# Optimization experiments

Measured on AMD Instinct MI355X. Metric: run time of the kernel, lower is better.

The kernel has to match this reference:

```python
import jax, jax.numpy as jnp
import numpy as np

B, N, DIM = 1, 4096, 512
HEADS, LOCAL_HEADS = 8, 4           # int(8*0.6)=4 local, 4 content
CONTENT_HEADS = HEADS - LOCAL_HEADS
HEAD_DIM = DIM // HEADS             # 64
WINDOW = 64                         # == H == W so window attention is well-formed
TOPK_RATIO = 0.2
SCALE = HEAD_DIM ** -0.5


def _window_partition(x, ws):
    Bb, H, W, C = x.shape
    pad_h = (ws - H % ws) % ws
    pad_w = (ws - W % ws) % ws
    x = jnp.pad(x, ((0, 0), (0, pad_h), (0, pad_w), (0, 0)))
    Hp, Wp = H + pad_h, W + pad_w
    x = x.reshape(Bb, Hp // ws, ws, Wp // ws, ws, C)
    win = x.transpose(0, 1, 3, 2, 4, 5).reshape(-1, ws, ws, C)
    return win, (Hp, Wp)


def _window_unpartition(win, ws, pad_hw, hw):
    Hp, Wp = pad_hw
    H, W = hw
    Bb = win.shape[0] // (Hp * Wp // ws // ws)
    x = win.reshape(Bb, Hp // ws, Wp // ws, ws, ws, -1)
    x = x.transpose(0, 1, 3, 2, 4, 5).reshape(Bb, Hp, Wp, -1)
    return x[:, :H, :W, :]


def setup_inputs() -> dict:
    key = jax.random.key(0)
    ks = jax.random.split(key, 12)
    s = 0.02
    f32 = jnp.float32
    ld = LOCAL_HEADS * HEAD_DIM      # 256
    cd = CONTENT_HEADS * HEAD_DIM    # 256
    return {
        'x': jax.random.normal(ks[0], (B, N, DIM), f32),
        'W_lqkv': jax.random.normal(ks[1], (DIM, 3 * ld), f32) * s,
        'b_lqkv': jnp.zeros((3 * ld,), f32),
        'W_cqkv': jax.random.normal(ks[2], (DIM, 3 * cd), f32) * s,
        'b_cqkv': jnp.zeros((3 * cd,), f32),
        'W_lproj': jax.random.normal(ks[3], (ld, DIM), f32) * s,
        'b_lproj': jnp.zeros((DIM,), f32),
        'W_cproj': jax.random.normal(ks[4], (cd, DIM), f32) * s,
        'b_cproj': jnp.zeros((DIM,), f32),
        'W_s1': jax.random.normal(ks[5], (DIM, DIM // 2), f32) * s,
        'b_s1': jnp.zeros((DIM // 2,), f32),
        'W_s2': jax.random.normal(ks[6], (DIM // 2, 1), f32) * s,
        'b_s2': jnp.zeros((1,), f32),
    }


def reference(x, W_lqkv, b_lqkv, W_cqkv, b_cqkv, W_lproj, b_lproj,
              W_cproj, b_cproj, W_s1, b_s1, W_s2, b_s2):
    Bb, Nn, C = x.shape
    H = W = int(np.sqrt(Nn))

    # ---- local (windowed) attention branch ----
    x_sp = x.reshape(Bb, H, W, C)
    x_win, pad_hw = _window_partition(x_sp, WINDOW)           # (Bw, ws, ws, C)
    Bw, Hw, Ww, _ = x_win.shape
    Nw = Hw * Ww
    xl = x_win.reshape(Bw, Nw, C)
    lqkv = (xl @ W_lqkv + b_lqkv).reshape(Bw, Nw, 3, LOCAL_HEADS, HEAD_DIM)
    lqkv = lqkv.transpose(2, 0, 3, 1, 4)                      # (3, Bw, h, Nw, d)
    lq, lk, lv = lqkv[0], lqkv[1], lqkv[2]
    lattn = jnp.einsum('bhqd,bhkd->bhqk', lq, lk) * SCALE
    lattn = jax.nn.softmax(lattn, axis=-1)
    lo = jnp.einsum('bhqk,bhkd->bhqd', lattn, lv)
    lo = lo.transpose(0, 2, 1, 3).reshape(Bw, Hw, Ww, LOCAL_HEADS * HEAD_DIM)
    lo = _window_unpartition(lo, WINDOW, pad_hw, (H, W)).reshape(Bb, Nn, -1)
    local_x = lo @ W_lproj + b_lproj

    # ---- saliency-gated content-based sparse attention branch ----
    h = jax.nn.gelu(x @ W_s1 + b_s1, approximate=False)
    scores = (h @ W_s2 + b_s2)[..., 0]                        # (B, N)
    K = max(1, int(Nn * TOPK_RATIO))
    _, idx = jax.lax.top_k(scores, K)                         # (B, K)
    mask = jnp.zeros((Bb, Nn), bool).at[jnp.arange(Bb)[:, None], idx].set(True)

    cqkv = (x @ W_cqkv + b_cqkv).reshape(Bb, Nn, 3, CONTENT_HEADS, HEAD_DIM)
    cqkv = cqkv.transpose(2, 0, 3, 1, 4)
    cq, ck, cv = cqkv[0], cqkv[1], cqkv[2]
    cattn = jnp.einsum('bhqd,bhkd->bhqk', cq, ck) * SCALE
    cattn = jnp.where(mask[:, None, None, :], cattn, -jnp.inf)
    cattn = jax.nn.softmax(cattn, axis=-1)
    co = jnp.einsum('bhqk,bhkd->bhqd', cattn, cv)
    co = co.transpose(0, 2, 1, 3).reshape(Bb, Nn, CONTENT_HEADS * HEAD_DIM)
    content_x = co @ W_cproj + b_cproj

    out = local_x + content_x
    attn = jnp.concatenate([lattn.mean(axis=1), cattn.mean(axis=1)], axis=1)
    return out, attn
```

## Files before the change

kernel.cpp:

```cpp
#include <hip/hip_runtime.h>

typedef __bf16 bf16;
typedef __bf16 bf16x4 __attribute__((ext_vector_type(4)));
typedef __bf16 bf16x8 __attribute__((ext_vector_type(8)));
typedef float  floatx4 __attribute__((ext_vector_type(4)));

__device__ __forceinline__ floatx4 mfma16(bf16x8 a, bf16x8 b, floatx4 c) {
    return __builtin_amdgcn_mfma_f32_16x16x32_bf16(a, b, c, 0, 0, 0);
}

__device__ __forceinline__ void transpose_tile(const float* __restrict__ src,
                                               bf16* __restrict__ dst,
                                               int R, int C, int rt, int ct,
                                               float (*tile)[33]) {
    int t = threadIdx.x;
    int tx = t & 31, ty = t >> 5;
    int c0 = ct * 32, r0 = rt * 32;
    for (int i = ty; i < 32; i += 8) {
        int r = r0 + i, c = c0 + tx;
        tile[i][tx] = (r < R && c < C) ? src[r * C + c] : 0.f;
    }
    __syncthreads();
    for (int i = ty; i < 32; i += 8) {
        int r = r0 + tx, c = c0 + i;
        if (r < R && c < C) dst[(size_t)c * R + r] = (bf16)tile[tx][i];
    }
}

__global__ __launch_bounds__(256) void k_prep(
    const float* __restrict__ W_lqkv, const float* __restrict__ W_cqkv,
    const float* __restrict__ x,
    bf16* __restrict__ WlT, bf16* __restrict__ WcT, bf16* __restrict__ xb)
{
    __shared__ float tile[32][33];
    int b = blockIdx.x;
    if (b < 384) {
        transpose_tile(W_lqkv, WlT, 512, 768, b / 24, b % 24, tile);
    } else if (b < 768) {
        transpose_tile(W_cqkv, WcT, 512, 768, (b - 384) / 24, (b - 384) % 24, tile);
    } else {
        int i = ((b - 768) * 256 + threadIdx.x) * 8;
        float4 f0 = *(const float4*)(x + i);
        float4 f1 = *(const float4*)(x + i + 4);
        bf16x8 a;
        a[0] = (bf16)f0.x; a[1] = (bf16)f0.y; a[2] = (bf16)f0.z; a[3] = (bf16)f0.w;
        a[4] = (bf16)f1.x; a[5] = (bf16)f1.y; a[6] = (bf16)f1.z; a[7] = (bf16)f1.w;
        *(bf16x8*)(xb + i) = a;
    }
}

__global__ __launch_bounds__(256) void k_qkv(
    const bf16* __restrict__ xb,
    const bf16* __restrict__ WlT, const bf16* __restrict__ WcT,
    const float* __restrict__ b_l, const float* __restrict__ b_c,
    bf16* __restrict__ lq, bf16* __restrict__ lk, bf16* __restrict__ lv,
    bf16* __restrict__ cq, bf16* __restrict__ ck, bf16* __restrict__ cv)
{
    const int tid = threadIdx.x;
    const int wave = tid >> 6, lane = tid & 63;
    const int ln15 = lane & 15, quad = lane >> 4;
    const int m0 = blockIdx.x * 64 + wave * 16;
    const int n0 = blockIdx.y * 64;

    floatx4 acc[4];
    for (int s = 0; s < 4; ++s) acc[s] = (floatx4){0.f, 0.f, 0.f, 0.f};

    for (int k0 = 0; k0 < 512; k0 += 32) {
        bf16x8 a = *(const bf16x8*)(xb + (m0 + ln15) * 512 + k0 + quad * 8);
        for (int s = 0; s < 4; ++s) {
            int cg = n0 + s * 16 + ln15;
            const bf16* bt = (cg < 768) ? (WlT + cg * 512) : (WcT + (cg - 768) * 512);
            bf16x8 b = *(const bf16x8*)(bt + k0 + quad * 8);
            acc[s] = mfma16(a, b, acc[s]);
        }
    }

    for (int s = 0; s < 4; ++s) {
        int cg = n0 + s * 16 + ln15;
        for (int r = 0; r < 4; ++r) {
            int row = m0 + quad * 4 + r;
            float v = acc[s][r];
            if (cg < 768) {
                v += b_l[cg];
                int qkv = cg >> 8, hh = (cg >> 6) & 3, d = cg & 63;
                if (qkv == 0)      lq[(hh * 4096 + row) * 64 + d] = (bf16)(v * 0.125f);
                else if (qkv == 1) lk[(hh * 4096 + row) * 64 + d] = (bf16)v;
                else               lv[(hh * 4096 + row) * 64 + d] = (bf16)v;
            } else {
                int c = cg - 768;
                v += b_c[c];
                int qkv = c >> 8, hh = (c >> 6) & 3, d = c & 63;
                if (qkv == 0)      cq[(hh * 4096 + row) * 64 + d] = (bf16)(v * 0.125f);
                else if (qkv == 1) ck[(hh * 4096 + row) * 64 + d] = (bf16)v;
                else               cv[(hh * 4096 + row) * 64 + d] = (bf16)v;
            }
        }
    }
}

__global__ __launch_bounds__(256) void k_scores(
    const float* __restrict__ x, const float* __restrict__ Ws1,
    const float* __restrict__ bs1, const float* __restrict__ Ws2,
    const float* __restrict__ bs2, float* __restrict__ scores)
{
    __shared__ float xs[16][512];
    int row0 = blockIdx.x * 16;
    int t = threadIdx.x;
    for (int i = t; i < 2048; i += 256) {
        int r = i >> 7, k4 = (i & 127) * 4;
        *(float4*)&xs[r][k4] = *(const float4*)&x[(row0 + r) * 512 + k4];
    }
    __syncthreads();
    int w = t >> 6, cb = (t & 63) * 4;
    float acc[4][4];
    #pragma unroll
    for (int rr = 0; rr < 4; ++rr)
        for (int j = 0; j < 4; ++j) acc[rr][j] = 0.f;
    #pragma unroll 2
    for (int k = 0; k < 512; ++k) {
        float4 wv = *(const float4*)(Ws1 + k * 256 + cb);
        #pragma unroll
        for (int rr = 0; rr < 4; ++rr) {
            float a = xs[w * 4 + rr][k];
            acc[rr][0] = fmaf(a, wv.x, acc[rr][0]);
            acc[rr][1] = fmaf(a, wv.y, acc[rr][1]);
            acc[rr][2] = fmaf(a, wv.z, acc[rr][2]);
            acc[rr][3] = fmaf(a, wv.w, acc[rr][3]);
        }
    }
    float b1[4] = {bs1[cb], bs1[cb + 1], bs1[cb + 2], bs1[cb + 3]};
    float w2[4] = {Ws2[cb], Ws2[cb + 1], Ws2[cb + 2], Ws2[cb + 3]};
    #pragma unroll
    for (int rr = 0; rr < 4; ++rr) {
        float s = 0.f;
        #pragma unroll
        for (int j = 0; j < 4; ++j) {
            float v = acc[rr][j] + b1[j];
            float g = 0.5f * v * (1.0f + erff(v * 0.70710678118654752f));
            s = fmaf(g, w2[j], s);
        }
        s += __shfl_xor(s, 1, 64);  s += __shfl_xor(s, 2, 64);
        s += __shfl_xor(s, 4, 64);  s += __shfl_xor(s, 8, 64);
        s += __shfl_xor(s, 16, 64); s += __shfl_xor(s, 32, 64);
        if ((t & 63) == 0) scores[row0 + w * 4 + rr] = s + bs2[0];
    }
}

__global__ __launch_bounds__(1024) void k_topk(const float* __restrict__ scores,
                                               int* __restrict__ sel, int* __restrict__ pos) {
    __shared__ unsigned ubuf[4096];
    __shared__ unsigned cga[2048], cgb[2048];
    __shared__ int bidx[1024];
    __shared__ int ctr, bctr, Bbin;
    int tid = threadIdx.x;
    if (tid == 0) { ctr = 0; bctr = 0; }
    for (int i = tid; i < 2048; i += 1024) cga[i] = 0u;
    __syncthreads();
    for (int i = tid; i < 4096; i += 1024) {
        unsigned s = __float_as_uint(scores[i]);
        unsigned u = (s & 0x80000000u) ? ~s : (s | 0x80000000u);
        ubuf[i] = u;
        pos[i] = -1;
        atomicAdd(&cga[u >> 21], 1u);
    }
    __syncthreads();
    unsigned* src = cga; unsigned* dst = cgb;
    for (int off = 1; off < 2048; off <<= 1) {
        for (int i = tid; i < 2048; i += 1024)
            dst[i] = src[i] + ((i + off < 2048) ? src[i + off] : 0u);
        __syncthreads();
        unsigned* tmp = src; src = dst; dst = tmp;
    }
    for (int b = tid; b < 2048; b += 1024) {
        unsigned ge = src[b];
        unsigned gt = (b < 2047) ? src[b + 1] : 0u;
        if (ge >= 819u && gt < 819u) Bbin = b;
    }
    __syncthreads();
    int B = Bbin;
    int countAbove = (B < 2047) ? (int)src[B + 1] : 0;
    int need = 819 - countAbove;
    for (int i = tid; i < 4096; i += 1024) {
        int b = (int)(ubuf[i] >> 21);
        if (b > B) {
            int slot = atomicAdd(&ctr, 1);
            sel[slot] = i;
            pos[i] = slot;
        } else if (b == B) {
            int ls = atomicAdd(&bctr, 1);
            if (ls < 1024) bidx[ls] = i;
        }
    }
    __syncthreads();
    int m = bctr;
    if (m <= 1024) {
        for (int e = tid; e < m; e += 1024) {
            int i = bidx[e];
            unsigned ui = ubuf[i];
            int rank = 0;
            for (int j = 0; j < m; ++j) {
                int ij = bidx[j];
                unsigned uj = ubuf[ij];
                rank += (uj > ui || (uj == ui && ij < i)) ? 1 : 0;
            }
            if (rank < need) { int slot = countAbove + rank; sel[slot] = i; pos[i] = slot; }
        }
    } else {
        for (int i = tid; i < 4096; i += 1024) {
            if ((int)(ubuf[i] >> 21) != B) continue;
            unsigned ui = ubuf[i];
            int rank = 0;
            for (int j = 0; j < 4096; ++j) {
                if ((int)(ubuf[j] >> 21) != B) continue;
                unsigned uj = ubuf[j];
                rank += (uj > ui || (uj == ui && j < i)) ? 1 : 0;
            }
            if (rank < need) { int slot = countAbove + rank; sel[slot] = i; pos[i] = slot; }
        }
    }
}

__global__ __launch_bounds__(256) void k_vt2(
    const bf16* __restrict__ lv, bf16* __restrict__ lvT,
    const bf16* __restrict__ ck, const bf16* __restrict__ cv,
    const int* __restrict__ sel,
    bf16* __restrict__ ckg, bf16* __restrict__ cvgT)
{
    __shared__ bf16 tile[64][66];
    int b = blockIdx.x;
    int t = threadIdx.x;
    int lane = t & 63, grp = t >> 6;
    if (b < 256) {
        int tr = b & 63, h = b >> 6;
        const bf16* s = lv + ((size_t)h * 4096 + tr * 64) * 64;
        #pragma unroll
        for (int rr = 0; rr < 16; ++rr) {
            int row = rr * 4 + grp;
            tile[row][lane] = s[row * 64 + lane];
        }
        __syncthreads();
        bf16* d = lvT + (size_t)h * 64 * 4096 + tr * 64;
        #pragma unroll
        for (int cc = 0; cc < 16; ++cc) {
            int col = cc * 4 + grp;
            d[(size_t)col * 4096 + lane] = tile[lane][col];
        }
    } else {
        int g = b - 256;
        int hh = g / 14, tl = g % 14;
        int r0 = tl * 64;
        #pragma unroll
        for (int rr = 0; rr < 16; ++rr) {
            int row = r0 + rr * 4 + grp;
            int src = (row < 819) ? sel[row] : -1;
            bf16 kv = (src >= 0) ? ck[(hh * 4096 + src) * 64 + lane] : (bf16)0.0f;
            bf16 vv = (src >= 0) ? cv[(hh * 4096 + src) * 64 + lane] : (bf16)0.0f;
            ckg[(hh * 896 + row) * 64 + lane] = kv;
            tile[rr * 4 + grp][lane] = vv;
        }
        __syncthreads();
        bf16* d = cvgT + (size_t)hh * 64 * 896 + r0;
        #pragma unroll
        for (int cc = 0; cc < 16; ++cc) {
            int col = cc * 4 + grp;
            d[(size_t)col * 896 + lane] = tile[lane][col];
        }
    }
}

__global__ __launch_bounds__(256, 5) void k_pass2b(
    const bf16* __restrict__ lq, const bf16* __restrict__ lk, const bf16* __restrict__ lvT,
    const bf16* __restrict__ cq, const bf16* __restrict__ ckg, const bf16* __restrict__ cvgT,
    float* __restrict__ partOL,
    float* __restrict__ partSL,
    float* __restrict__ lsum,
    bf16* __restrict__ cob)
{
    __shared__ __align__(16) bf16 pbuf[4][2][16 * 40];
    int wave = threadIdx.x >> 6, lane = threadIdx.x & 63;
    int ln15 = lane & 15, quad = lane >> 4;
    int m0 = blockIdx.x * 64 + wave * 16;
    int y = blockIdx.y;
    bool local = y < 16;
    int h     = local ? (y >> 2) : (y - 16);
    int split = local ? (y & 3) : 0;
    int NV    = local ? 4096 : 896;
    int kbeg  = local ? split * 1024 : 0;
    int kcnt  = local ? 1024 : 896;

    const bf16* Qh = (local ? lq : cq) + (h * 4096 + m0) * 64;
    const bf16* Kh = (local ? lk : ckg) + h * NV * 64;
    const bf16* Vh = (local ? lvT : cvgT) + h * 64 * NV;

    bf16x8 af0 = *(const bf16x8*)(Qh + ln15 * 64 + quad * 8);
    bf16x8 af1 = *(const bf16x8*)(Qh + ln15 * 64 + 32 + quad * 8);

    floatx4 o[4];
    #pragma unroll
    for (int ds = 0; ds < 4; ++ds) o[ds] = (floatx4){0.f, 0.f, 0.f, 0.f};
    float se[4] = {0.f, 0.f, 0.f, 0.f};

    for (int key0 = kbeg; key0 < kbeg + kcnt; key0 += 64) {
        #pragma unroll
        for (int c = 0; c < 2; ++c) {
            int kb = key0 + c * 32;
            bf16* pb = &pbuf[wave][c][0];
            #pragma unroll
            for (int s = 0; s < 2; ++s) {
                int kc = kb + s * 16;
                const bf16* krow = Kh + (kc + ln15) * 64;
                floatx4 z0 = (floatx4){0.f, 0.f, 0.f, 0.f};
                floatx4 z1 = (floatx4){0.f, 0.f, 0.f, 0.f};
                z0 = mfma16(af0, *(const bf16x8*)(krow + quad * 8), z0);
                z1 = mfma16(af1, *(const bf16x8*)(krow + 32 + quad * 8), z1);
                bool valid = local || (kc + ln15) < 819;
                #pragma unroll
                for (int r = 0; r < 4; ++r) {
                    float p = valid ? __expf(fminf(z0[r] + z1[r], 60.f)) : 0.0f;
                    se[r] += p;
                    pb[(quad * 4 + r) * 40 + s * 16 + ln15] = (bf16)p;
                }
            }
        }
        #pragma unroll
        for (int c = 0; c < 2; ++c) {
            int kb = key0 + c * 32;
            bf16x8 ap = *(const bf16x8*)(&pbuf[wave][c][0] + ln15 * 40 + quad * 8);
            #pragma unroll
            for (int ds = 0; ds < 4; ++ds) {
                const bf16* vrow = Vh + (ds * 16 + ln15) * NV + kb + quad * 8;
                o[ds] = mfma16(ap, *(const bf16x8*)vrow, o[ds]);
            }
        }
    }

    if (local) {
        float* ps = partSL + (split * 4 + h) * 4096;
        #pragma unroll
        for (int r = 0; r < 4; ++r) {
            float s = se[r];
            s += __shfl_xor(s, 1, 64);
            s += __shfl_xor(s, 2, 64);
            s += __shfl_xor(s, 4, 64);
            s += __shfl_xor(s, 8, 64);
            if (ln15 == 0) ps[m0 + quad * 4 + r] = s;
        }
        float* ob = partOL + (size_t)split * (4096 * 256);
        #pragma unroll
        for (int ds = 0; ds < 4; ++ds)
            for (int r = 0; r < 4; ++r)
                ob[(m0 + quad * 4 + r) * 256 + h * 64 + ds * 16 + ln15] = o[ds][r];
    } else {
        float rl[4];
        #pragma unroll
        for (int r = 0; r < 4; ++r) {
            float s = se[r];
            s += __shfl_xor(s, 1, 64);
            s += __shfl_xor(s, 2, 64);
            s += __shfl_xor(s, 4, 64);
            s += __shfl_xor(s, 8, 64);
            if (ln15 == 0) lsum[(4 + h) * 4096 + m0 + quad * 4 + r] = s;
            rl[r] = 1.0f / fmaxf(s, 1e-30f);
        }
        #pragma unroll
        for (int ds = 0; ds < 4; ++ds)
            for (int r = 0; r < 4; ++r)
                cob[(m0 + quad * 4 + r) * 256 + h * 64 + ds * 16 + ln15] =
                    (bf16)(o[ds][r] * rl[r]);
    }
}

__global__ __launch_bounds__(256) void k_reduce2(
    const float* __restrict__ partOL, const float* __restrict__ partSL,
    float* __restrict__ lsum, bf16* __restrict__ lob)
{
    int t = threadIdx.x;
    int q0 = blockIdx.x * 4;
    int r = t >> 6, cc = (t & 63) * 4;
    int q = q0 + r;
    int h = cc >> 6;

    float sl = 0.f;
    #pragma unroll
    for (int s = 0; s < 4; ++s) sl += partSL[(s * 4 + h) * 4096 + q];
    float rll = 1.0f / fmaxf(sl, 1e-30f);
    float a0 = 0.f, a1 = 0.f, a2 = 0.f, a3 = 0.f;
    #pragma unroll
    for (int s = 0; s < 4; ++s) {
        float4 v = *(const float4*)(partOL + (size_t)s * 1048576 + q * 256 + cc);
        a0 += v.x; a1 += v.y; a2 += v.z; a3 += v.w;
    }
    bf16x4 ol;
    ol[0] = (bf16)(a0 * rll); ol[1] = (bf16)(a1 * rll);
    ol[2] = (bf16)(a2 * rll); ol[3] = (bf16)(a3 * rll);
    *(bf16x4*)(lob + q * 256 + cc) = ol;

    if (t < 16) {
        int h8 = t >> 2, rr = t & 3, qq = q0 + rr;
        float s = 0.f;
        #pragma unroll
        for (int sp = 0; sp < 4; ++sp) s += partSL[(sp * 4 + h8) * 4096 + qq];
        lsum[h8 * 4096 + qq] = s;
    }
}

__global__ __launch_bounds__(256) void k_pass2a(
    const bf16* __restrict__ lq, const bf16* __restrict__ lk,
    const bf16* __restrict__ cq, const bf16* __restrict__ ckg,
    const float* __restrict__ lsum,
    float* __restrict__ attn_local,
    bf16* __restrict__ pcomp)
{
    int wave = threadIdx.x >> 6, lane = threadIdx.x & 63;
    int ln15 = lane & 15, quad = lane >> 4;
    int m0 = blockIdx.x * 64 + wave * 16;
    int y = blockIdx.y;
    bool local = y < 16;
    const bf16* Q  = local ? lq : cq;
    const bf16* Kt = local ? lk : ckg;
    int NV = local ? 4096 : 896;
    int kbeg = local ? y * 256 : (y - 16) * 224;
    int kend = kbeg + (local ? 256 : 224);
    int hbase = local ? 0 : 4;

    bf16x8 af[4][2];
    #pragma unroll
    for (int h2 = 0; h2 < 4; ++h2)
        for (int ks = 0; ks < 2; ++ks)
            af[h2][ks] = *(const bf16x8*)(Q + (h2 * 4096 + m0 + ln15) * 64 + ks * 32 + quad * 8);

    float rl[4][4];
    #pragma unroll
    for (int h2 = 0; h2 < 4; ++h2)
        for (int r = 0; r < 4; ++r)
            rl[h2][r] = 0.25f / fmaxf(lsum[(hbase + h2) * 4096 + m0 + quad * 4 + r], 1e-30f);

    for (int key0 = kbeg; key0 < kend; key0 += 32) {
        float pm[2][4] = {{0.f, 0.f, 0.f, 0.f}, {0.f, 0.f, 0.f, 0.f}};
        #pragma unroll
        for (int h2 = 0; h2 < 4; ++h2) {
            #pragma unroll
            for (int s = 0; s < 2; ++s) {
                int kc = key0 + s * 16;
                const bf16* krow = Kt + (h2 * NV + kc + ln15) * 64;
                floatx4 z0 = (floatx4){0.f, 0.f, 0.f, 0.f};
                floatx4 z1 = (floatx4){0.f, 0.f, 0.f, 0.f};
                z0 = mfma16(af[h2][0], *(const bf16x8*)(krow + quad * 8), z0);
                z1 = mfma16(af[h2][1], *(const bf16x8*)(krow + 32 + quad * 8), z1);
                bool valid = local || (kc + ln15) < 819;
                if (valid)
                    for (int r = 0; r < 4; ++r)
                        pm[s][r] += __expf(fminf(z0[r] + z1[r], 60.f)) * rl[h2][r];
            }
        }
        if (local) {
            #pragma unroll
            for (int s = 0; s < 2; ++s)
                for (int r = 0; r < 4; ++r)
                    attn_local[(m0 + quad * 4 + r) * 4096 + key0 + s * 16 + ln15] = pm[s][r];
        } else {
            #pragma unroll
            for (int s = 0; s < 2; ++s) {
                int kc = key0 + s * 16 + ln15;
                if (kc < 832)
                    for (int r = 0; r < 4; ++r)
                        pcomp[(m0 + quad * 4 + r) * 832 + kc] = (bf16)(pm[s][r]);
            }
        }
    }
}

__global__ __launch_bounds__(256) void k_expand2(
    const bf16* __restrict__ pcomp, const int* __restrict__ pos,
    const float* __restrict__ W_lproj, const float* __restrict__ W_cproj,
    bf16* __restrict__ WlpT, bf16* __restrict__ WcpT,
    float* __restrict__ attn_content)
{
    __shared__ float tile[32][33];
    int b = blockIdx.x;
    if (b < 4096) {
        int c0 = threadIdx.x * 16;
        const bf16* prow = pcomp + b * 832;
        float vals[16];
        #pragma unroll
        for (int j = 0; j < 16; ++j) {
            int p = pos[c0 + j];
            vals[j] = (p >= 0) ? (float)prow[p] : 0.0f;
        }
        float* dst = attn_content + (size_t)b * 4096 + c0;
        *(float4*)(dst)      = (float4){vals[0], vals[1], vals[2], vals[3]};
        *(float4*)(dst + 4)  = (float4){vals[4], vals[5], vals[6], vals[7]};
        *(float4*)(dst + 8)  = (float4){vals[8], vals[9], vals[10], vals[11]};
        *(float4*)(dst + 12) = (float4){vals[12], vals[13], vals[14], vals[15]};
    } else if (b < 4224) {
        int g = b - 4096;
        transpose_tile(W_lproj, WlpT, 256, 512, g / 16, g % 16, tile);
    } else {
        int g = b - 4224;
        transpose_tile(W_cproj, WcpT, 256, 512, g / 16, g % 16, tile);
    }
}

__global__ __launch_bounds__(256) void k_proj(
    const bf16* __restrict__ lob, const bf16* __restrict__ cob,
    const bf16* __restrict__ WlpT, const bf16* __restrict__ WcpT,
    const float* __restrict__ bl, const float* __restrict__ bc,
    float* __restrict__ out)
{
    const int tid = threadIdx.x;
    const int wave = tid >> 6, lane = tid & 63;
    const int ln15 = lane & 15, quad = lane >> 4;
    const int m0 = blockIdx.x * 64 + wave * 16;
    const int n0 = blockIdx.y * 32;

    floatx4 acc[2];
    acc[0] = (floatx4){0.f, 0.f, 0.f, 0.f};
    acc[1] = (floatx4){0.f, 0.f, 0.f, 0.f};

    for (int k0 = 0; k0 < 256; k0 += 32) {
        bf16x8 al = *(const bf16x8*)(lob + (m0 + ln15) * 256 + k0 + quad * 8);
        bf16x8 ac = *(const bf16x8*)(cob + (m0 + ln15) * 256 + k0 + quad * 8);
        #pragma unroll
        for (int s = 0; s < 2; ++s) {
            int c = n0 + s * 16 + ln15;
            acc[s] = mfma16(al, *(const bf16x8*)(WlpT + c * 256 + k0 + quad * 8), acc[s]);
            acc[s] = mfma16(ac, *(const bf16x8*)(WcpT + c * 256 + k0 + quad * 8), acc[s]);
        }
    }
    #pragma unroll
    for (int s = 0; s < 2; ++s) {
        int c = n0 + s * 16 + ln15;
        float bias = bl[c] + bc[c];
        for (int r = 0; r < 4; ++r)
            out[(m0 + quad * 4 + r) * 512 + c] = acc[s][r] + bias;
    }
}

#define OFF_WLQKVT  0L
#define OFF_WCQKVT  786432L
#define OFF_LQ      1572864L
#define OFF_LK      3670016L
#define OFF_LVT     5767168L
#define OFF_CQ      7864320L
#define OFF_CK      9961472L
#define OFF_CV      12058624L
#define OFF_PCOMP   9961472L
#define OFF_CKG     16777216L
#define OFF_CVGT    17235968L
#define OFF_WLPT    16777216L
#define OFF_WCPT    17039360L
#define OFF_SCORES  17694720L
#define OFF_SEL     17711104L
#define OFF_POS     17715200L
#define OFF_LSUM    17731584L
#define OFF_LO      17862656L
#define OFF_CO      22056960L
#define WS_TOTAL    26251264L

extern "C" void kernel_launch(void* const* d_in, const int* in_sizes, int n_in,
                              void* d_out, int out_size, void* d_ws, size_t ws_size,
                              hipStream_t stream) {
    if (ws_size < (size_t)WS_TOTAL) return;

    const float* x       = (const float*)d_in[0];
    const float* W_lqkv  = (const float*)d_in[1];
    const float* b_lqkv  = (const float*)d_in[2];
    const float* W_cqkv  = (const float*)d_in[3];
    const float* b_cqkv  = (const float*)d_in[4];
    const float* W_lproj = (const float*)d_in[5];
    const float* b_lproj = (const float*)d_in[6];
    const float* W_cproj = (const float*)d_in[7];
    const float* b_cproj = (const float*)d_in[8];
    const float* W_s1    = (const float*)d_in[9];
    const float* b_s1    = (const float*)d_in[10];
    const float* W_s2    = (const float*)d_in[11];
    const float* b_s2    = (const float*)d_in[12];

    char* ws = (char*)d_ws;
    bf16* WlqkvT  = (bf16*)(ws + OFF_WLQKVT);
    bf16* WcqkvT  = (bf16*)(ws + OFF_WCQKVT);
    bf16* lq    = (bf16*)(ws + OFF_LQ);
    bf16* lk    = (bf16*)(ws + OFF_LK);
    bf16* lvT   = (bf16*)(ws + OFF_LVT);
    bf16* cq    = (bf16*)(ws + OFF_CQ);
    bf16* ck    = (bf16*)(ws + OFF_CK);
    bf16* cv    = (bf16*)(ws + OFF_CV);
    bf16* pcomp = (bf16*)(ws + OFF_PCOMP);
    bf16* ckg   = (bf16*)(ws + OFF_CKG);
    bf16* cvgT  = (bf16*)(ws + OFF_CVGT);
    bf16* WlpT  = (bf16*)(ws + OFF_WLPT);
    bf16* WcpT  = (bf16*)(ws + OFF_WCPT);
    float* scores  = (float*)(ws + OFF_SCORES);
    int*   sel     = (int*)(ws + OFF_SEL);
    int*   pos     = (int*)(ws + OFF_POS);
    float* lsum    = (float*)(ws + OFF_LSUM);
    bf16*  xb      = (bf16*)(ws + OFF_LO);
    bf16*  lob     = (bf16*)(ws + OFF_LO);
    bf16*  lv      = (bf16*)(ws + OFF_CO);
    bf16*  cob     = (bf16*)(ws + OFF_CO);

    float* outp = (float*)d_out;
    float* attn_local   = outp + 2097152;
    float* attn_content = attn_local + 4096 * 4096;
    float* partOL = attn_content;
    float* partSL = attn_content + 4194304;

    k_prep<<<1792, 256, 0, stream>>>(W_lqkv, W_cqkv, x, WlqkvT, WcqkvT, xb);
    k_qkv<<<dim3(64, 24), 256, 0, stream>>>(xb, WlqkvT, WcqkvT, b_lqkv, b_cqkv,
                                            lq, lk, lv, cq, ck, cv);
    k_scores<<<256, 256, 0, stream>>>(x, W_s1, b_s1, W_s2, b_s2, scores);
    k_topk<<<1, 1024, 0, stream>>>(scores, sel, pos);
    k_vt2<<<312, 256, 0, stream>>>(lv, lvT, ck, cv, sel, ckg, cvgT);
    k_pass2b<<<dim3(64, 20), 256, 0, stream>>>(lq, lk, lvT, cq, ckg, cvgT,
                                               partOL, partSL, lsum, cob);
    k_reduce2<<<1024, 256, 0, stream>>>(partOL, partSL, lsum, lob);
    k_pass2a<<<dim3(64, 20), 256, 0, stream>>>(lq, lk, cq, ckg, lsum,
                                               attn_local, pcomp);
    k_expand2<<<4352, 256, 0, stream>>>(pcomp, pos, W_lproj, W_cproj,
                                        WlpT, WcpT, attn_content);
    k_proj<<<dim3(64, 16), 256, 0, stream>>>(lob, cob, WlpT, WcpT, b_lproj, b_cproj, outp);
}
```

Measured before the change: 657.9 us.

## Process two query tiles per wave in attention pass and split keys eightfold

Each wave in k_pass2b now handles two 16-row query tiles, so every loaded K and V fragment feeds two MFMAs and global key/value traffic per query is halved. To keep the grid full, the local branch's key dimension is split into 8 chunks of 512 instead of 4 of 1024, and the reduction kernel sums 8 partials. This doubles the partial-output scratch written and read through the attn_content buffer, and raises per-thread register use and LDS per block.

```diff
diff --git a/kernel.cpp b/kernel.cpp
--- a/kernel.cpp
+++ b/kernel.cpp
@@ -276,60 +276,72 @@
     float* __restrict__ lsum,
     bf16* __restrict__ cob)
 {
-    __shared__ __align__(16) bf16 pbuf[4][2][16 * 40];
+    __shared__ __align__(16) bf16 pbuf[4][2][2][16 * 40];
     int wave = threadIdx.x >> 6, lane = threadIdx.x & 63;
     int ln15 = lane & 15, quad = lane >> 4;
-    int m0 = blockIdx.x * 64 + wave * 16;
+    int m0 = blockIdx.x * 128 + wave * 16;
     int y = blockIdx.y;
-    bool local = y < 16;
-    int h     = local ? (y >> 2) : (y - 16);
-    int split = local ? (y & 3) : 0;
+    bool local = y < 32;
+    int h     = local ? (y >> 3) : (y - 32);
+    int split = local ? (y & 7) : 0;
     int NV    = local ? 4096 : 896;
-    int kbeg  = local ? split * 1024 : 0;
-    int kcnt  = local ? 1024 : 896;
-
-    const bf16* Qh = (local ? lq : cq) + (h * 4096 + m0) * 64;
+    int kbeg  = local ? split * 512 : 0;
+    int kcnt  = local ? 512 : 896;
+
+    const bf16* Qb = (local ? lq : cq) + h * 4096 * 64;
     const bf16* Kh = (local ? lk : ckg) + h * NV * 64;
     const bf16* Vh = (local ? lvT : cvgT) + h * 64 * NV;
 
-    bf16x8 af0 = *(const bf16x8*)(Qh + ln15 * 64 + quad * 8);
-    bf16x8 af1 = *(const bf16x8*)(Qh + ln15 * 64 + 32 + quad * 8);
-
-    floatx4 o[4];
-    #pragma unroll
-    for (int ds = 0; ds < 4; ++ds) o[ds] = (floatx4){0.f, 0.f, 0.f, 0.f};
-    float se[4] = {0.f, 0.f, 0.f, 0.f};
+    bf16x8 af[2][2];
+    #pragma unroll
+    for (int mt = 0; mt < 2; ++mt) {
+        af[mt][0] = *(const bf16x8*)(Qb + (m0 + mt * 64 + ln15) * 64 + quad * 8);
+        af[mt][1] = *(const bf16x8*)(Qb + (m0 + mt * 64 + ln15) * 64 + 32 + quad * 8);
+    }
+
+    floatx4 o[2][4];
+    #pragma unroll
+    for (int mt = 0; mt < 2; ++mt)
+        for (int ds = 0; ds < 4; ++ds) o[mt][ds] = (floatx4){0.f, 0.f, 0.f, 0.f};
+    float se[2][4] = {{0.f, 0.f, 0.f, 0.f}, {0.f, 0.f, 0.f, 0.f}};
 
     for (int key0 = kbeg; key0 < kbeg + kcnt; key0 += 64) {
         #pragma unroll
         for (int c = 0; c < 2; ++c) {
             int kb = key0 + c * 32;
-            bf16* pb = &pbuf[wave][c][0];
             #pragma unroll
             for (int s = 0; s < 2; ++s) {
                 int kc = kb + s * 16;
                 const bf16* krow = Kh + (kc + ln15) * 64;
-                floatx4 z0 = (floatx4){0.f, 0.f, 0.f, 0.f};
-                floatx4 z1 = (floatx4){0.f, 0.f, 0.f, 0.f};
-                z0 = mfma16(af0, *(const bf16x8*)(krow + quad * 8), z0);
-                z1 = mfma16(af1, *(const bf16x8*)(krow + 32 + quad * 8), z1);
+                bf16x8 b0 = *(const bf16x8*)(krow + quad * 8);
+                bf16x8 b1 = *(const bf16x8*)(krow + 32 + quad * 8);
                 bool valid = local || (kc + ln15) < 819;
                 #pragma unroll
-                for (int r = 0; r < 4; ++r) {
-                    float p = valid ? __expf(fminf(z0[r] + z1[r], 60.f)) : 0.0f;
-                    se[r] += p;
-                    pb[(quad * 4 + r) * 40 + s * 16 + ln15] = (bf16)p;
+                for (int mt = 0; mt < 2; ++mt) {
+                    floatx4 z0 = (floatx4){0.f, 0.f, 0.f, 0.f};
+                    floatx4 z1 = (floatx4){0.f, 0.f, 0.f, 0.f};
+                    z0 = mfma16(af[mt][0], b0, z0);
+                    z1 = mfma16(af[mt][1], b1, z1);
+                    bf16* pb = &pbuf[wave][mt][c][0];
+                    #pragma unroll
+                    for (int r = 0; r < 4; ++r) {
+                        float p = valid ? __expf(fminf(z0[r] + z1[r], 60.f)) : 0.0f;
+                        se[mt][r] += p;
+                        pb[(quad * 4 + r) * 40 + s * 16 + ln15] = (bf16)p;
+                    }
                 }
             }
         }
         #pragma unroll
         for (int c = 0; c < 2; ++c) {
             int kb = key0 + c * 32;
-            bf16x8 ap = *(const bf16x8*)(&pbuf[wave][c][0] + ln15 * 40 + quad * 8);
+            bf16x8 ap0 = *(const bf16x8*)(&pbuf[wave][0][c][0] + ln15 * 40 + quad * 8);
+            bf16x8 ap1 = *(const bf16x8*)(&pbuf[wave][1][c][0] + ln15 * 40 + quad * 8);
             #pragma unroll
             for (int ds = 0; ds < 4; ++ds) {
-                const bf16* vrow = Vh + (ds * 16 + ln15) * NV + kb + quad * 8;
-                o[ds] = mfma16(ap, *(const bf16x8*)vrow, o[ds]);
+                bf16x8 vb = *(const bf16x8*)(Vh + (ds * 16 + ln15) * NV + kb + quad * 8);
+                o[0][ds] = mfma16(ap0, vb, o[0][ds]);
+                o[1][ds] = mfma16(ap1, vb, o[1][ds]);
             }
         }
     }
@@ -337,36 +349,42 @@
     if (local) {
         float* ps = partSL + (split * 4 + h) * 4096;
         #pragma unroll
-        for (int r = 0; r < 4; ++r) {
-            float s = se[r];
-            s += __shfl_xor(s, 1, 64);
-            s += __shfl_xor(s, 2, 64);
-            s += __shfl_xor(s, 4, 64);
-            s += __shfl_xor(s, 8, 64);
-            if (ln15 == 0) ps[m0 + quad * 4 + r] = s;
-        }
+        for (int mt = 0; mt < 2; ++mt)
+            for (int r = 0; r < 4; ++r) {
+                float s = se[mt][r];
+                s += __shfl_xor(s, 1, 64);
+                s += __shfl_xor(s, 2, 64);
+                s += __shfl_xor(s, 4, 64);
+                s += __shfl_xor(s, 8, 64);
+                if (ln15 == 0) ps[m0 + mt * 64 + quad * 4 + r] = s;
+            }
         float* ob = partOL + (size_t)split * (4096 * 256);
         #pragma unroll
-        for (int ds = 0; ds < 4; ++ds)
-            for (int r = 0; r < 4; ++r)
-                ob[(m0 + quad * 4 + r) * 256 + h * 64 + ds * 16 + ln15] = o[ds][r];
+        for (int mt = 0; mt < 2; ++mt)
+            for (int ds = 0; ds < 4; ++ds)
+                for (int r = 0; r < 4; ++r)
+                    ob[(m0 + mt * 64 + quad * 4 + r) * 256 + h * 64 + ds * 16 + ln15] =
+                        o[mt][ds][r];
     } else {
-        float rl[4];
-        #pragma unroll
-        for (int r = 0; r < 4; ++r) {
-            float s = se[r];
-            s += __shfl_xor(s, 1, 64);
-            s += __shfl_xor(s, 2, 64);
-            s += __shfl_xor(s, 4, 64);
-            s += __shfl_xor(s, 8, 64);
-            if (ln15 == 0) lsum[(4 + h) * 4096 + m0 + quad * 4 + r] = s;
-            rl[r] = 1.0f / fmaxf(s, 1e-30f);
-        }
-        #pragma unroll
-        for (int ds = 0; ds < 4; ++ds)
-            for (int r = 0; r < 4; ++r)
-                cob[(m0 + quad * 4 + r) * 256 + h * 64 + ds * 16 + ln15] =
-                    (bf16)(o[ds][r] * rl[r]);
+        #pragma unroll
+        for (int mt = 0; mt < 2; ++mt) {
+            float rl[4];
+            #pragma unroll
+            for (int r = 0; r < 4; ++r) {
+                float s = se[mt][r];
+                s += __shfl_xor(s, 1, 64);
+                s += __shfl_xor(s, 2, 64);
+                s += __shfl_xor(s, 4, 64);
+                s += __shfl_xor(s, 8, 64);
+                if (ln15 == 0) lsum[(4 + h) * 4096 + m0 + mt * 64 + quad * 4 + r] = s;
+                rl[r] = 1.0f / fmaxf(s, 1e-30f);
+            }
+            #pragma unroll
+            for (int ds = 0; ds < 4; ++ds)
+                for (int r = 0; r < 4; ++r)
+                    cob[(m0 + mt * 64 + quad * 4 + r) * 256 + h * 64 + ds * 16 + ln15] =
+                        (bf16)(o[mt][ds][r] * rl[r]);
+        }
     }
 }
 
@@ -382,11 +400,11 @@
 
     float sl = 0.f;
     #pragma unroll
-    for (int s = 0; s < 4; ++s) sl += partSL[(s * 4 + h) * 4096 + q];
+    for (int s = 0; s < 8; ++s) sl += partSL[(s * 4 + h) * 4096 + q];
     float rll = 1.0f / fmaxf(sl, 1e-30f);
     float a0 = 0.f, a1 = 0.f, a2 = 0.f, a3 = 0.f;
     #pragma unroll
-    for (int s = 0; s < 4; ++s) {
+    for (int s = 0; s < 8; ++s) {
         float4 v = *(const float4*)(partOL + (size_t)s * 1048576 + q * 256 + cc);
         a0 += v.x; a1 += v.y; a2 += v.z; a3 += v.w;
     }
@@ -399,7 +417,7 @@
         int h8 = t >> 2, rr = t & 3, qq = q0 + rr;
         float s = 0.f;
         #pragma unroll
-        for (int sp = 0; sp < 4; ++sp) s += partSL[(sp * 4 + h8) * 4096 + qq];
+        for (int sp = 0; sp < 8; ++sp) s += partSL[(sp * 4 + h8) * 4096 + qq];
         lsum[h8 * 4096 + qq] = s;
     }
 }
@@ -603,7 +621,7 @@
     float* attn_local   = outp + 2097152;
     float* attn_content = attn_local + 4096 * 4096;
     float* partOL = attn_content;
-    float* partSL = attn_content + 4194304;
+    float* partSL = attn_content + 8388608;
 
     k_prep<<<1792, 256, 0, stream>>>(W_lqkv, W_cqkv, x, WlqkvT, WcqkvT, xb);
     k_qkv<<<dim3(64, 24), 256, 0, stream>>>(xb, WlqkvT, WcqkvT, b_lqkv, b_cqkv,
@@ -611,7 +629,7 @@
     k_scores<<<256, 256, 0, stream>>>(x, W_s1, b_s1, W_s2, b_s2, scores);
     k_topk<<<1, 1024, 0, stream>>>(scores, sel, pos);
     k_vt2<<<312, 256, 0, stream>>>(lv, lvT, ck, cv, sel, ckg, cvgT);
-    k_pass2b<<<dim3(64, 20), 256, 0, stream>>>(lq, lk, lvT, cq, ckg, cvgT,
+    k_pass2b<<<dim3(32, 36), 256, 0, stream>>>(lq, lk, lvT, cq, ckg, cvgT,
                                                partOL, partSL, lsum, cob);
     k_reduce2<<<1024, 256, 0, stream>>>(partOL, partSL, lsum, lob);
     k_pass2a<<<dim3(64, 20), 256, 0, stream>>>(lq, lk, cq, ckg, lsum,
```

Result: no change. 659.7 us (+0.3%).
